# Kernel optimization log

Measured on AMD Instinct MI355X. Metric: run time of the kernel, lower is better.

## Reference

```python
import jax, jax.numpy as jnp
import numpy as np

MARGIN = 5.0
VAR_FLOOR = 1e-4
BIG = 1e6


def setup_inputs() -> dict:
    key = jax.random.key(0)
    ks = jax.random.split(key, 8)
    B, D, R = 512, 768, 128
    C_new, C_old = 10, 100
    return {
        "features": jax.random.normal(ks[0], (B, D), jnp.float32),
        "labels": jax.random.randint(ks[1], (B,), 0, C_new),
        "new_class_ids": jnp.arange(C_new),
        "cur_means": jax.random.normal(ks[2], (C_new, D), jnp.float32),
        "cur_bases": jax.random.normal(ks[3], (C_new, D, R), jnp.float32),
        "cur_variances": jax.random.uniform(ks[4], (C_new, R + 1), jnp.float32),
        "calibrated_old_means": jax.random.normal(ks[5], (C_old, D), jnp.float32),
        "calibrated_old_bases": jax.random.normal(ks[6], (C_old, D, R), jnp.float32),
        "calibrated_old_variances": jax.random.uniform(ks[7], (C_old, R + 1), jnp.float32),
    }


def _geometry_distance_matrix(z, means, bases, variances):
    # z: [B,D], means: [C,D], bases: [C,D,R], variances: [C,R+1] -> [B,C]
    diff = z[:, None, :] - means[None, :, :]                    # [B,C,D]
    coeff = jnp.einsum('bcd,cdr->bcr', diff, bases)             # [B,C,R]
    eig = jnp.maximum(variances[:, :-1], VAR_FLOOR)             # [C,R]
    res = jnp.maximum(variances[:, -1], VAR_FLOOR)              # [C]
    parallel = jnp.sum(coeff * coeff / eig[None, :, :], axis=-1)  # [B,C]
    recon = jnp.einsum('bcr,cdr->bcd', coeff, bases)            # [B,C,D]
    residual_term = jnp.sum((diff - recon) ** 2, axis=-1) / res[None, :]
    dist = (parallel + residual_term) / z.shape[1]              # normalize_by_dim
    return jnp.nan_to_num(dist, nan=BIG, posinf=BIG, neginf=BIG)


def reference(features, labels, new_class_ids, cur_means, cur_bases, cur_variances,
              calibrated_old_means, calibrated_old_bases, calibrated_old_variances):
    z = jnp.nan_to_num(features, nan=0.0, posinf=0.0, neginf=0.0)  # [B,D]
    labels = labels.reshape(-1)

    own_all = _geometry_distance_matrix(z, cur_means, cur_bases, cur_variances)  # [B,C_new_total]
    old_all = _geometry_distance_matrix(z, calibrated_old_means, calibrated_old_bases,
                                        calibrated_old_variances)               # [B,C_old]
    old_min = jnp.min(old_all, axis=1)                                           # [B]

    # Per-new-class masks; union of class masks reproduces new_mask implicitly.
    masks = (labels[None, :] == new_class_ids[:, None]).astype(z.dtype)          # [K,B]
    counts = masks.sum(axis=1)                                                   # [K]
    denom = jnp.maximum(counts, 1.0)

    own_k = own_all[:, new_class_ids].T                                          # [K,B]
    hinge = jax.nn.relu(MARGIN + own_k - old_min[None, :])                       # [K,B]

    total_k = (hinge * masks).sum(axis=1) / denom
    own_k_mean = (own_k * masks).sum(axis=1) / denom
    old_k_mean = (old_min[None, :] * masks).sum(axis=1) / denom

    valid = (counts > 0).astype(z.dtype)
    n_valid = jnp.maximum(valid.sum(), 1.0)
    total = (total_k * valid).sum() / n_valid
    own = (own_k_mean * valid).sum() / n_valid
    old = (old_k_mean * valid).sum() / n_valid
    return jnp.stack([total, own, old])  # [total, own, old]
```

## Files before the change

kernel.cpp:

```cpp
#include <hip/hip_runtime.h>
#include <hip/hip_bf16.h>
#include <math.h>
#include <stdint.h>

#define B_N   512
#define D_N   768
#define R_N   128
#define C_NEW 10
#define C_OLD 100
#define C_TOT 110
#define MARGIN_F    5.0f
#define VAR_FLOOR_F 1e-4f
#define BIG_F       1e6f

typedef __bf16 bf16;
typedef __bf16 bf16x4 __attribute__((ext_vector_type(4)));
typedef __bf16 bf16x8 __attribute__((ext_vector_type(8)));
typedef float  f32x4  __attribute__((ext_vector_type(4)));

__device__ __forceinline__ float cleanf(float v) { return isfinite(v) ? v : 0.0f; }

__device__ __forceinline__ unsigned encf(float f) {
    unsigned u = __float_as_uint(f);
    return (u & 0x80000000u) ? ~u : (u | 0x80000000u);
}
__device__ __forceinline__ float decf(unsigned u) {
    return (u & 0x80000000u) ? __uint_as_float(u & 0x7fffffffu) : __uint_as_float(~u);
}

__global__ __launch_bounds__(256)
void prep_T(const float* __restrict__ cur_bases, const float* __restrict__ old_bases,
            bf16* __restrict__ basesT, unsigned* __restrict__ ominE,
            unsigned* __restrict__ cnt)
{
    const int bid = blockIdx.x, t = threadIdx.x;
    if (bid == 0) {
        ominE[t] = 0xFFFFFFFFu;
        ominE[256 + t] = 0xFFFFFFFFu;
        if (t == 0) *cnt = 0u;
    }

    const int dt = bid % 6, c = bid / 6;
    const float* Bc = (c < C_NEW) ? cur_bases + (size_t)c * D_N * R_N
                                  : old_bases + (size_t)(c - C_NEW) * D_N * R_N;
    __shared__ bf16 T[128][128];
    const int d0 = dt * 128;
    const int rg  = t & 31;
    const int dgb = t >> 5;

    #pragma unroll
    for (int i = 0; i < 4; ++i) {
        const int dg = i * 8 + dgb;
        const float* src = Bc + (size_t)(d0 + dg * 4) * R_N + rg * 4;
        float4 v0 = *(const float4*)(src);
        float4 v1 = *(const float4*)(src + R_N);
        float4 v2 = *(const float4*)(src + 2 * R_N);
        float4 v3 = *(const float4*)(src + 3 * R_N);
        const float* f0 = (const float*)&v0;
        const float* f1 = (const float*)&v1;
        const float* f2 = (const float*)&v2;
        const float* f3 = (const float*)&v3;
        #pragma unroll
        for (int j = 0; j < 4; ++j) {
            const int R = rg * 4 + j;
            const int pc = dg ^ (R & 31);
            bf16x4 w;
            w[0] = (bf16)f0[j]; w[1] = (bf16)f1[j]; w[2] = (bf16)f2[j]; w[3] = (bf16)f3[j];
            *(bf16x4*)(&T[R][pc * 4]) = w;
        }
    }
    __syncthreads();

    #pragma unroll
    for (int it = 0; it < 16; ++it) {
        const int q = it * 256 + t;
        const int r = q >> 5, u = q & 31;
        const int pc = u ^ (r & 31);
        ushort4 w = *(const ushort4*)(&T[r][pc * 4]);
        *(ushort4*)(basesT + (size_t)c * R_N * D_N + (size_t)r * D_N + d0 + u * 4) = w;
    }
}

#define PADC 136
#define SM_A   0
#define SM_B   18432
#define SM_C   0
#define SM_G   36864
#define SM_MU  71680
#define SM_INV 74752
#define SM_Q   75264
#define SM_PAR 75776
#define SM_CN  76288
#define SM_ND  76800
#define SM_T2  77312
#define SM_FL  79360
#define SM_SZ  79376

__global__ __launch_bounds__(256, 2)
void main_all(const float* __restrict__ z, const bf16* __restrict__ basesT,
              const float* __restrict__ cur_vars, const float* __restrict__ old_vars,
              const float* __restrict__ cur_means, const float* __restrict__ old_means,
              const int* __restrict__ labels, const int* __restrict__ ncid,
              float* __restrict__ gdist, unsigned* __restrict__ ominE,
              unsigned* __restrict__ cnt, float* __restrict__ out)
{
    __shared__ __align__(16) unsigned char smem[SM_SZ];
    bf16*  sA   = (bf16*)(smem + SM_A);
    bf16*  sB   = (bf16*)(smem + SM_B);
    bf16*  sC   = (bf16*)(smem + SM_C);
    bf16*  sG   = (bf16*)(smem + SM_G);
    float* sMu  = (float*)(smem + SM_MU);
    float* sInv = (float*)(smem + SM_INV);
    float* sQ   = (float*)(smem + SM_Q);
    float* sPar = (float*)(smem + SM_PAR);
    float* sCn  = (float*)(smem + SM_CN);
    float* sNd  = (float*)(smem + SM_ND);
    float* sT2  = (float*)(smem + SM_T2);
    unsigned* sFl = (unsigned*)(smem + SM_FL);

    const int tid = threadIdx.x, wave = tid >> 6, lane = tid & 63;
    const int quad = lane >> 4, l15 = lane & 15;
    const int wr = (wave >> 1) * 64, wc = (wave & 1) * 64;

    const int fid = blockIdx.x;
    const int c  = (fid & 7) + 8 * (fid >> 5);
    const int mt = (fid >> 3) & 3;

    if (c < C_TOT) {
        const int b0 = mt * 128;
        const float* vars = (c < C_NEW) ? cur_vars + (size_t)c * (R_N + 1)
                                        : old_vars + (size_t)(c - C_NEW) * (R_N + 1);
        const float* mu = (c < C_NEW) ? cur_means + (size_t)c * D_N
                                      : old_means + (size_t)(c - C_NEW) * D_N;

        if (tid < 128) {
            sInv[tid] = 1.0f / fmaxf(vars[tid], VAR_FLOOR_F);
            sQ[tid] = 0.0f;
        }
        for (int i = tid; i < D_N; i += 256) sMu[i] = mu[i];

        f32x4 acc1[4][4], accG[4][4];
        #pragma unroll
        for (int i = 0; i < 4; ++i)
            #pragma unroll
            for (int j = 0; j < 4; ++j) { acc1[i][j] = (f32x4)0.0f; accG[i][j] = (f32x4)0.0f; }
        float nd2p[8];
        #pragma unroll
        for (int p = 0; p < 8; ++p) nd2p[p] = 0.f;

        const int rb = tid >> 4, f4 = tid & 15;
        const float* Az = z + (size_t)b0 * D_N;
        const bf16*  Bb = basesT + (size_t)c * R_N * D_N;

        for (int k0 = 0; k0 < D_N; k0 += 64) {
            __syncthreads();
            #pragma unroll
            for (int p = 0; p < 4; ++p) {
                int q = p * 256 + tid, row = q >> 3, u = q & 7;
                *(uint4*)(sB + row * 72 + u * 8) = *(const uint4*)(Bb + (size_t)row * D_N + k0 + u * 8);
            }
            {
                float4 m4 = *(const float4*)(sMu + k0 + f4 * 4);
                #pragma unroll
                for (int p = 0; p < 8; ++p) {
                    int row = p * 16 + rb;
                    float4 v = *(const float4*)(Az + (size_t)row * D_N + k0 + f4 * 4);
                    float d0 = cleanf(v.x) - m4.x;
                    float d1 = cleanf(v.y) - m4.y;
                    float d2 = cleanf(v.z) - m4.z;
                    float d3 = cleanf(v.w) - m4.w;
                    nd2p[p] += d0 * d0 + d1 * d1 + d2 * d2 + d3 * d3;
                    bf16x4 w;
                    w[0] = (bf16)d0; w[1] = (bf16)d1; w[2] = (bf16)d2; w[3] = (bf16)d3;
                    *(bf16x4*)(sA + row * 72 + f4 * 4) = w;
                }
            }
            __syncthreads();
            #pragma unroll
            for (int kk = 0; kk < 64; kk += 32) {
                bf16x8 afA[4], bgB[4], afB[4];
                #pragma unroll
                for (int i = 0; i < 4; ++i) afA[i] = *(const bf16x8*)(sA + (wr + 16 * i + l15) * 72 + kk + quad * 8);
                #pragma unroll
                for (int j = 0; j < 4; ++j) bgB[j] = *(const bf16x8*)(sB + (wc + 16 * j + l15) * 72 + kk + quad * 8);
                #pragma unroll
                for (int i = 0; i < 4; ++i) afB[i] = *(const bf16x8*)(sB + (wr + 16 * i + l15) * 72 + kk + quad * 8);
                #pragma unroll
                for (int i = 0; i < 4; ++i)
                    #pragma unroll
                    for (int j = 0; j < 4; ++j) {
                        acc1[i][j] = __builtin_amdgcn_mfma_f32_16x16x32_bf16(afA[i], bgB[j], acc1[i][j], 0, 0, 0);
                        accG[i][j] = __builtin_amdgcn_mfma_f32_16x16x32_bf16(afB[i], bgB[j], accG[i][j], 0, 0, 0);
                    }
            }
        }

        #pragma unroll
        for (int p = 0; p < 8; ++p) {
            float s = nd2p[p];
            s += __shfl_xor(s, 1, 64); s += __shfl_xor(s, 2, 64);
            s += __shfl_xor(s, 4, 64); s += __shfl_xor(s, 8, 64);
            if (l15 == 0) sNd[p * 16 + rb] = s;
        }

        #pragma unroll
        for (int i = 0; i < 4; ++i)
            #pragma unroll
            for (int j = 0; j < 4; ++j)
                #pragma unroll
                for (int reg = 0; reg < 4; ++reg)
                    sG[(wr + 16 * i + quad * 4 + reg) * PADC + wc + 16 * j + l15] = (bf16)accG[i][j][reg];
        __syncthreads();

        #pragma unroll
        for (int i = 0; i < 4; ++i)
            #pragma unroll
            for (int j = 0; j < 4; ++j)
                #pragma unroll
                for (int reg = 0; reg < 4; ++reg)
                    sC[(wr + 16 * i + quad * 4 + reg) * PADC + wc + 16 * j + l15] = (bf16)acc1[i][j][reg];
        __syncthreads();

        {
            int row = tid >> 1, half = tid & 1;
            float par = 0.f, cn = 0.f;
            #pragma unroll
            for (int m = 0; m < 8; ++m) {
                bf16x8 v = *(const bf16x8*)(sC + row * PADC + half * 64 + m * 8);
                #pragma unroll
                for (int e = 0; e < 8; ++e) {
                    float f = (float)v[e];
                    int col = half * 64 + m * 8 + e;
                    cn  += f * f;
                    par += f * f * sInv[col];
                }
            }
            sT2[tid] = par;
            sT2[256 + tid] = cn;
        }
        __syncthreads();
        if (tid < 128) {
            sPar[tid] = sT2[tid * 2] + sT2[tid * 2 + 1];
            sCn[tid]  = sT2[256 + tid * 2] + sT2[256 + tid * 2 + 1];
        }

        f32x4 acc2[4][4];
        #pragma unroll
        for (int i = 0; i < 4; ++i)
            #pragma unroll
            for (int j = 0; j < 4; ++j) acc2[i][j] = (f32x4)0.0f;
        #pragma unroll
        for (int kc = 0; kc < 128; kc += 32) {
            bf16x8 af[4], bg[4];
            #pragma unroll
            for (int i = 0; i < 4; ++i) af[i] = *(const bf16x8*)(sC + (wr + 16 * i + l15) * PADC + kc + quad * 8);
            #pragma unroll
            for (int j = 0; j < 4; ++j) bg[j] = *(const bf16x8*)(sG + (wc + 16 * j + l15) * PADC + kc + quad * 8);
            #pragma unroll
            for (int i = 0; i < 4; ++i)
                #pragma unroll
                for (int j = 0; j < 4; ++j)
                    acc2[i][j] = __builtin_amdgcn_mfma_f32_16x16x32_bf16(af[i], bg[j], acc2[i][j], 0, 0, 0);
        }

        #pragma unroll
        for (int i = 0; i < 4; ++i)
            #pragma unroll
            for (int reg = 0; reg < 4; ++reg) {
                float qp = 0.f;
                #pragma unroll
                for (int j = 0; j < 4; ++j) qp += acc2[i][j][reg] * acc1[i][j][reg];
                qp += __shfl_xor(qp, 1, 64);
                qp += __shfl_xor(qp, 2, 64);
                qp += __shfl_xor(qp, 4, 64);
                qp += __shfl_xor(qp, 8, 64);
                if (l15 == 0) atomicAdd(&sQ[wr + 16 * i + quad * 4 + reg], qp);
            }
        __syncthreads();

        if (tid < 128) {
            int b = b0 + tid;
            float res = fmaxf(vars[R_N], VAR_FLOOR_F);
            float dist = (sPar[tid] + (sNd[tid] - 2.0f * sCn[tid] + sQ[tid]) / res) / (float)D_N;
            if (!isfinite(dist)) dist = BIG_F;
            if (c < C_NEW) {
                gdist[(size_t)b * C_NEW + c] = dist;
            } else {
                atomicMin(ominE + b, encf(dist));
            }
        }
    }

    __syncthreads();
    if (tid == 0) {
        __threadfence();
        sFl[0] = atomicAdd(cnt, 1u);
    }
    __syncthreads();
    if (sFl[0] == 447u) {
        __threadfence();
        float* accF = sT2;
        int* ncidS = (int*)(sT2 + 48);
        if (tid < 40) accF[tid] = 0.f;
        if (tid < C_NEW) ncidS[tid] = ncid[tid];
        __syncthreads();
        #pragma unroll
        for (int rep = 0; rep < 2; ++rep) {
            int b = rep * 256 + tid;
            float mn = decf(ominE[b]);
            int lab = labels[b];
            #pragma unroll
            for (int k = 0; k < C_NEW; ++k) {
                if (lab == ncidS[k]) {
                    int col = min(max(ncidS[k], 0), C_NEW - 1);
                    float ow = gdist[(size_t)b * C_NEW + col];
                    atomicAdd(&accF[k * 4 + 0], 1.0f);
                    atomicAdd(&accF[k * 4 + 1], fmaxf(0.0f, MARGIN_F + ow - mn));
                    atomicAdd(&accF[k * 4 + 2], ow);
                    atomicAdd(&accF[k * 4 + 3], mn);
                }
            }
        }
        __syncthreads();
        if (tid == 0) {
            float total = 0.f, own = 0.f, old = 0.f, nv = 0.f;
            #pragma unroll
            for (int k = 0; k < C_NEW; ++k) {
                float cntk = accF[k * 4 + 0];
                float den = fmaxf(cntk, 1.0f);
                if (cntk > 0.f) {
                    nv += 1.f;
                    total += accF[k * 4 + 1] / den;
                    own   += accF[k * 4 + 2] / den;
                    old   += accF[k * 4 + 3] / den;
                }
            }
            float nvd = fmaxf(nv, 1.0f);
            out[0] = total / nvd;
            out[1] = own / nvd;
            out[2] = old / nvd;
        }
    }
}

extern "C" void kernel_launch(void* const* d_in, const int* in_sizes, int n_in,
                              void* d_out, int out_size, void* d_ws, size_t ws_size,
                              hipStream_t stream)
{
    const float* features  = (const float*)d_in[0];
    const int*   labels    = (const int*)d_in[1];
    const int*   ncid      = (const int*)d_in[2];
    const float* cur_means = (const float*)d_in[3];
    const float* cur_bases = (const float*)d_in[4];
    const float* cur_vars  = (const float*)d_in[5];
    const float* old_means = (const float*)d_in[6];
    const float* old_bases = (const float*)d_in[7];
    const float* old_vars  = (const float*)d_in[8];

    unsigned char* ws = (unsigned char*)d_ws;
    float*    gdist  = (float*)(ws + 0);
    unsigned* ominE  = (unsigned*)(ws + 20480);
    unsigned* cnt    = (unsigned*)(ws + 22528);
    bf16*     basesT = (bf16*) (ws + 22544);

    prep_T<<<dim3(6 * C_TOT), dim3(256), 0, stream>>>(cur_bases, old_bases,
                                                      basesT, ominE, cnt);
    main_all<<<dim3(448), dim3(256), 0, stream>>>(features, basesT,
                                                  cur_vars, old_vars,
                                                  cur_means, old_means,
                                                  labels, ncid,
                                                  gdist, ominE, cnt, (float*)d_out);
}
```

Measured before the change: 165.5 us.

## Split Gram and projection GEMM loops with register prefetch; move finalize to separate kernel

The fused K loop that computed both the projection (diff·B) and the Gram matrix (BᵀB) is split into two sequential 12-step loops. Each loop prefetches the next chunk of bases and features into registers while the current chunk is in shared memory, so global loads overlap the MFMA work. The last-block atomic counter reduction is replaced by a separate single-block finalize kernel, and blocks with no class now return early. Running two loops reads the bases tile twice and holds more live registers for the prefetch buffers, which may reduce occupancy under launch_bounds(256,2), and it adds one kernel launch.

```diff
diff --git a/kernel.cpp b/kernel.cpp
--- a/kernel.cpp
+++ b/kernel.cpp
@@ -30,14 +30,12 @@
 
 __global__ __launch_bounds__(256)
 void prep_T(const float* __restrict__ cur_bases, const float* __restrict__ old_bases,
-            bf16* __restrict__ basesT, unsigned* __restrict__ ominE,
-            unsigned* __restrict__ cnt)
+            bf16* __restrict__ basesT, unsigned* __restrict__ ominE)
 {
     const int bid = blockIdx.x, t = threadIdx.x;
     if (bid == 0) {
         ominE[t] = 0xFFFFFFFFu;
         ominE[256 + t] = 0xFFFFFFFFu;
-        if (t == 0) *cnt = 0u;
     }
 
     const int dt = bid % 6, c = bid / 6;
@@ -93,17 +91,19 @@
 #define SM_CN  76288
 #define SM_ND  76800
 #define SM_T2  77312
-#define SM_FL  79360
-#define SM_SZ  79376
+#define SM_SZ  79360
 
 __global__ __launch_bounds__(256, 2)
 void main_all(const float* __restrict__ z, const bf16* __restrict__ basesT,
               const float* __restrict__ cur_vars, const float* __restrict__ old_vars,
               const float* __restrict__ cur_means, const float* __restrict__ old_means,
-              const int* __restrict__ labels, const int* __restrict__ ncid,
-              float* __restrict__ gdist, unsigned* __restrict__ ominE,
-              unsigned* __restrict__ cnt, float* __restrict__ out)
+              float* __restrict__ gdist, unsigned* __restrict__ ominE)
 {
+    const int fid = blockIdx.x;
+    const int c  = (fid & 7) + 8 * (fid >> 5);
+    const int mt = (fid >> 3) & 3;
+    if (c >= C_TOT) return;
+
     __shared__ __align__(16) unsigned char smem[SM_SZ];
     bf16*  sA   = (bf16*)(smem + SM_A);
     bf16*  sB   = (bf16*)(smem + SM_B);
@@ -116,230 +116,288 @@
     float* sCn  = (float*)(smem + SM_CN);
     float* sNd  = (float*)(smem + SM_ND);
     float* sT2  = (float*)(smem + SM_T2);
-    unsigned* sFl = (unsigned*)(smem + SM_FL);
 
     const int tid = threadIdx.x, wave = tid >> 6, lane = tid & 63;
     const int quad = lane >> 4, l15 = lane & 15;
     const int wr = (wave >> 1) * 64, wc = (wave & 1) * 64;
 
-    const int fid = blockIdx.x;
-    const int c  = (fid & 7) + 8 * (fid >> 5);
-    const int mt = (fid >> 3) & 3;
-
-    if (c < C_TOT) {
-        const int b0 = mt * 128;
-        const float* vars = (c < C_NEW) ? cur_vars + (size_t)c * (R_N + 1)
-                                        : old_vars + (size_t)(c - C_NEW) * (R_N + 1);
-        const float* mu = (c < C_NEW) ? cur_means + (size_t)c * D_N
-                                      : old_means + (size_t)(c - C_NEW) * D_N;
-
-        if (tid < 128) {
-            sInv[tid] = 1.0f / fmaxf(vars[tid], VAR_FLOOR_F);
-            sQ[tid] = 0.0f;
-        }
-        for (int i = tid; i < D_N; i += 256) sMu[i] = mu[i];
-
-        f32x4 acc1[4][4], accG[4][4];
-        #pragma unroll
-        for (int i = 0; i < 4; ++i)
-            #pragma unroll
-            for (int j = 0; j < 4; ++j) { acc1[i][j] = (f32x4)0.0f; accG[i][j] = (f32x4)0.0f; }
-        float nd2p[8];
-        #pragma unroll
-        for (int p = 0; p < 8; ++p) nd2p[p] = 0.f;
-
-        const int rb = tid >> 4, f4 = tid & 15;
-        const float* Az = z + (size_t)b0 * D_N;
-        const bf16*  Bb = basesT + (size_t)c * R_N * D_N;
-
-        for (int k0 = 0; k0 < D_N; k0 += 64) {
-            __syncthreads();
+    const int b0 = mt * 128;
+    const float* vars = (c < C_NEW) ? cur_vars + (size_t)c * (R_N + 1)
+                                    : old_vars + (size_t)(c - C_NEW) * (R_N + 1);
+    const float* mu = (c < C_NEW) ? cur_means + (size_t)c * D_N
+                                  : old_means + (size_t)(c - C_NEW) * D_N;
+
+    if (tid < 128) {
+        sInv[tid] = 1.0f / fmaxf(vars[tid], VAR_FLOOR_F);
+        sQ[tid] = 0.0f;
+    }
+    for (int i = tid; i < D_N; i += 256) sMu[i] = mu[i];
+
+    const int srow = (tid * 8) >> 6 , dummy = srow;
+    (void)dummy;
+    const int qrow = tid >> 3 << 0;
+    (void)qrow;
+
+    const bf16* Bb = basesT + (size_t)c * R_N * D_N;
+    const float* Az = z + (size_t)b0 * D_N;
+    const int rb = tid >> 4, f4 = tid & 15;
+
+    f32x4 accG[4][4];
+    #pragma unroll
+    for (int i = 0; i < 4; ++i)
+        #pragma unroll
+        for (int j = 0; j < 4; ++j) accG[i][j] = (f32x4)0.0f;
+
+    uint4 pb[4];
+    #pragma unroll
+    for (int p = 0; p < 4; ++p) {
+        int q = p * 256 + tid, row = q >> 3, u = q & 7;
+        pb[p] = *(const uint4*)(Bb + (size_t)row * D_N + 0 + u * 8);
+    }
+
+    for (int kc = 0; kc < 12; ++kc) {
+        __syncthreads();
+        #pragma unroll
+        for (int p = 0; p < 4; ++p) {
+            int q = p * 256 + tid, row = q >> 3, u = q & 7;
+            *(uint4*)(sB + row * 72 + u * 8) = pb[p];
+        }
+        if (kc < 11) {
             #pragma unroll
             for (int p = 0; p < 4; ++p) {
                 int q = p * 256 + tid, row = q >> 3, u = q & 7;
-                *(uint4*)(sB + row * 72 + u * 8) = *(const uint4*)(Bb + (size_t)row * D_N + k0 + u * 8);
-            }
-            {
-                float4 m4 = *(const float4*)(sMu + k0 + f4 * 4);
-                #pragma unroll
-                for (int p = 0; p < 8; ++p) {
-                    int row = p * 16 + rb;
-                    float4 v = *(const float4*)(Az + (size_t)row * D_N + k0 + f4 * 4);
-                    float d0 = cleanf(v.x) - m4.x;
-                    float d1 = cleanf(v.y) - m4.y;
-                    float d2 = cleanf(v.z) - m4.z;
-                    float d3 = cleanf(v.w) - m4.w;
-                    nd2p[p] += d0 * d0 + d1 * d1 + d2 * d2 + d3 * d3;
-                    bf16x4 w;
-                    w[0] = (bf16)d0; w[1] = (bf16)d1; w[2] = (bf16)d2; w[3] = (bf16)d3;
-                    *(bf16x4*)(sA + row * 72 + f4 * 4) = w;
-                }
-            }
-            __syncthreads();
-            #pragma unroll
-            for (int kk = 0; kk < 64; kk += 32) {
-                bf16x8 afA[4], bgB[4], afB[4];
-                #pragma unroll
-                for (int i = 0; i < 4; ++i) afA[i] = *(const bf16x8*)(sA + (wr + 16 * i + l15) * 72 + kk + quad * 8);
-                #pragma unroll
-                for (int j = 0; j < 4; ++j) bgB[j] = *(const bf16x8*)(sB + (wc + 16 * j + l15) * 72 + kk + quad * 8);
-                #pragma unroll
-                for (int i = 0; i < 4; ++i) afB[i] = *(const bf16x8*)(sB + (wr + 16 * i + l15) * 72 + kk + quad * 8);
-                #pragma unroll
-                for (int i = 0; i < 4; ++i)
-                    #pragma unroll
-                    for (int j = 0; j < 4; ++j) {
-                        acc1[i][j] = __builtin_amdgcn_mfma_f32_16x16x32_bf16(afA[i], bgB[j], acc1[i][j], 0, 0, 0);
-                        accG[i][j] = __builtin_amdgcn_mfma_f32_16x16x32_bf16(afB[i], bgB[j], accG[i][j], 0, 0, 0);
-                    }
-            }
-        }
-
-        #pragma unroll
-        for (int p = 0; p < 8; ++p) {
-            float s = nd2p[p];
-            s += __shfl_xor(s, 1, 64); s += __shfl_xor(s, 2, 64);
-            s += __shfl_xor(s, 4, 64); s += __shfl_xor(s, 8, 64);
-            if (l15 == 0) sNd[p * 16 + rb] = s;
-        }
-
-        #pragma unroll
-        for (int i = 0; i < 4; ++i)
-            #pragma unroll
-            for (int j = 0; j < 4; ++j)
-                #pragma unroll
-                for (int reg = 0; reg < 4; ++reg)
-                    sG[(wr + 16 * i + quad * 4 + reg) * PADC + wc + 16 * j + l15] = (bf16)accG[i][j][reg];
+                pb[p] = *(const uint4*)(Bb + (size_t)row * D_N + (kc + 1) * 64 + u * 8);
+            }
+        }
         __syncthreads();
-
-        #pragma unroll
-        for (int i = 0; i < 4; ++i)
-            #pragma unroll
-            for (int j = 0; j < 4; ++j)
-                #pragma unroll
-                for (int reg = 0; reg < 4; ++reg)
-                    sC[(wr + 16 * i + quad * 4 + reg) * PADC + wc + 16 * j + l15] = (bf16)acc1[i][j][reg];
-        __syncthreads();
-
-        {
-            int row = tid >> 1, half = tid & 1;
-            float par = 0.f, cn = 0.f;
-            #pragma unroll
-            for (int m = 0; m < 8; ++m) {
-                bf16x8 v = *(const bf16x8*)(sC + row * PADC + half * 64 + m * 8);
-                #pragma unroll
-                for (int e = 0; e < 8; ++e) {
-                    float f = (float)v[e];
-                    int col = half * 64 + m * 8 + e;
-                    cn  += f * f;
-                    par += f * f * sInv[col];
-                }
-            }
-            sT2[tid] = par;
-            sT2[256 + tid] = cn;
-        }
-        __syncthreads();
-        if (tid < 128) {
-            sPar[tid] = sT2[tid * 2] + sT2[tid * 2 + 1];
-            sCn[tid]  = sT2[256 + tid * 2] + sT2[256 + tid * 2 + 1];
-        }
-
-        f32x4 acc2[4][4];
-        #pragma unroll
-        for (int i = 0; i < 4; ++i)
-            #pragma unroll
-            for (int j = 0; j < 4; ++j) acc2[i][j] = (f32x4)0.0f;
-        #pragma unroll
-        for (int kc = 0; kc < 128; kc += 32) {
-            bf16x8 af[4], bg[4];
-            #pragma unroll
-            for (int i = 0; i < 4; ++i) af[i] = *(const bf16x8*)(sC + (wr + 16 * i + l15) * PADC + kc + quad * 8);
-            #pragma unroll
-            for (int j = 0; j < 4; ++j) bg[j] = *(const bf16x8*)(sG + (wc + 16 * j + l15) * PADC + kc + quad * 8);
+        #pragma unroll
+        for (int kk = 0; kk < 64; kk += 32) {
+            bf16x8 afB[4], bgB[4];
+            #pragma unroll
+            for (int i = 0; i < 4; ++i) afB[i] = *(const bf16x8*)(sB + (wr + 16 * i + l15) * 72 + kk + quad * 8);
+            #pragma unroll
+            for (int j = 0; j < 4; ++j) bgB[j] = *(const bf16x8*)(sB + (wc + 16 * j + l15) * 72 + kk + quad * 8);
             #pragma unroll
             for (int i = 0; i < 4; ++i)
                 #pragma unroll
                 for (int j = 0; j < 4; ++j)
-                    acc2[i][j] = __builtin_amdgcn_mfma_f32_16x16x32_bf16(af[i], bg[j], acc2[i][j], 0, 0, 0);
-        }
-
+                    accG[i][j] = __builtin_amdgcn_mfma_f32_16x16x32_bf16(afB[i], bgB[j], accG[i][j], 0, 0, 0);
+        }
+    }
+    #pragma unroll
+    for (int i = 0; i < 4; ++i)
+        #pragma unroll
+        for (int j = 0; j < 4; ++j)
+            #pragma unroll
+            for (int reg = 0; reg < 4; ++reg)
+                sG[(wr + 16 * i + quad * 4 + reg) * PADC + wc + 16 * j + l15] = (bf16)accG[i][j][reg];
+
+    f32x4 acc1[4][4];
+    #pragma unroll
+    for (int i = 0; i < 4; ++i)
+        #pragma unroll
+        for (int j = 0; j < 4; ++j) acc1[i][j] = (f32x4)0.0f;
+    float nd2p[8];
+    #pragma unroll
+    for (int p = 0; p < 8; ++p) nd2p[p] = 0.f;
+
+    float4 pa[8];
+    #pragma unroll
+    for (int p = 0; p < 4; ++p) {
+        int q = p * 256 + tid, row = q >> 3, u = q & 7;
+        pb[p] = *(const uint4*)(Bb + (size_t)row * D_N + 0 + u * 8);
+    }
+    #pragma unroll
+    for (int p = 0; p < 8; ++p) {
+        int row = p * 16 + rb;
+        pa[p] = *(const float4*)(Az + (size_t)row * D_N + 0 + f4 * 4);
+    }
+
+    for (int kc = 0; kc < 12; ++kc) {
+        const int k0 = kc * 64;
+        __syncthreads();
+        #pragma unroll
+        for (int p = 0; p < 4; ++p) {
+            int q = p * 256 + tid, row = q >> 3, u = q & 7;
+            *(uint4*)(sB + row * 72 + u * 8) = pb[p];
+        }
+        {
+            float4 m4 = *(const float4*)(sMu + k0 + f4 * 4);
+            #pragma unroll
+            for (int p = 0; p < 8; ++p) {
+                int row = p * 16 + rb;
+                float d0 = cleanf(pa[p].x) - m4.x;
+                float d1 = cleanf(pa[p].y) - m4.y;
+                float d2 = cleanf(pa[p].z) - m4.z;
+                float d3 = cleanf(pa[p].w) - m4.w;
+                nd2p[p] += d0 * d0 + d1 * d1 + d2 * d2 + d3 * d3;
+                bf16x4 w;
+                w[0] = (bf16)d0; w[1] = (bf16)d1; w[2] = (bf16)d2; w[3] = (bf16)d3;
+                *(bf16x4*)(sA + row * 72 + f4 * 4) = w;
+            }
+        }
+        if (kc < 11) {
+            #pragma unroll
+            for (int p = 0; p < 4; ++p) {
+                int q = p * 256 + tid, row = q >> 3, u = q & 7;
+                pb[p] = *(const uint4*)(Bb + (size_t)row * D_N + (kc + 1) * 64 + u * 8);
+            }
+            #pragma unroll
+            for (int p = 0; p < 8; ++p) {
+                int row = p * 16 + rb;
+                pa[p] = *(const float4*)(Az + (size_t)row * D_N + (kc + 1) * 64 + f4 * 4);
+            }
+        }
+        __syncthreads();
+        #pragma unroll
+        for (int kk = 0; kk < 64; kk += 32) {
+            bf16x8 afA[4], bgB[4];
+            #pragma unroll
+            for (int i = 0; i < 4; ++i) afA[i] = *(const bf16x8*)(sA + (wr + 16 * i + l15) * 72 + kk + quad * 8);
+            #pragma unroll
+            for (int j = 0; j < 4; ++j) bgB[j] = *(const bf16x8*)(sB + (wc + 16 * j + l15) * 72 + kk + quad * 8);
+            #pragma unroll
+            for (int i = 0; i < 4; ++i)
+                #pragma unroll
+                for (int j = 0; j < 4; ++j)
+                    acc1[i][j] = __builtin_amdgcn_mfma_f32_16x16x32_bf16(afA[i], bgB[j], acc1[i][j], 0, 0, 0);
+        }
+    }
+
+    #pragma unroll
+    for (int p = 0; p < 8; ++p) {
+        float s = nd2p[p];
+        s += __shfl_xor(s, 1, 64); s += __shfl_xor(s, 2, 64);
+        s += __shfl_xor(s, 4, 64); s += __shfl_xor(s, 8, 64);
+        if (l15 == 0) sNd[p * 16 + rb] = s;
+    }
+    __syncthreads();
+
+    #pragma unroll
+    for (int i = 0; i < 4; ++i)
+        #pragma unroll
+        for (int j = 0; j < 4; ++j)
+            #pragma unroll
+            for (int reg = 0; reg < 4; ++reg)
+                sC[(wr + 16 * i + quad * 4 + reg) * PADC + wc + 16 * j + l15] = (bf16)acc1[i][j][reg];
+    __syncthreads();
+
+    {
+        int row = tid >> 1, half = tid & 1;
+        float par = 0.f, cn = 0.f;
+        #pragma unroll
+        for (int m = 0; m < 8; ++m) {
+            bf16x8 v = *(const bf16x8*)(sC + row * PADC + half * 64 + m * 8);
+            #pragma unroll
+            for (int e = 0; e < 8; ++e) {
+                float f = (float)v[e];
+                int col = half * 64 + m * 8 + e;
+                cn  += f * f;
+                par += f * f * sInv[col];
+            }
+        }
+        sT2[tid] = par;
+        sT2[256 + tid] = cn;
+    }
+    __syncthreads();
+    if (tid < 128) {
+        sPar[tid] = sT2[tid * 2] + sT2[tid * 2 + 1];
+        sCn[tid]  = sT2[256 + tid * 2] + sT2[256 + tid * 2 + 1];
+    }
+
+    f32x4 acc2[4][4];
+    #pragma unroll
+    for (int i = 0; i < 4; ++i)
+        #pragma unroll
+        for (int j = 0; j < 4; ++j) acc2[i][j] = (f32x4)0.0f;
+    #pragma unroll
+    for (int kc = 0; kc < 128; kc += 32) {
+        bf16x8 af[4], bg[4];
+        #pragma unroll
+        for (int i = 0; i < 4; ++i) af[i] = *(const bf16x8*)(sC + (wr + 16 * i + l15) * PADC + kc + quad * 8);
+        #pragma unroll
+        for (int j = 0; j < 4; ++j) bg[j] = *(const bf16x8*)(sG + (wc + 16 * j + l15) * PADC + kc + quad * 8);
         #pragma unroll
         for (int i = 0; i < 4; ++i)
             #pragma unroll
-            for (int reg = 0; reg < 4; ++reg) {
-                float qp = 0.f;
-                #pragma unroll
-                for (int j = 0; j < 4; ++j) qp += acc2[i][j][reg] * acc1[i][j][reg];
-                qp += __shfl_xor(qp, 1, 64);
-                qp += __shfl_xor(qp, 2, 64);
-                qp += __shfl_xor(qp, 4, 64);
-                qp += __shfl_xor(qp, 8, 64);
-                if (l15 == 0) atomicAdd(&sQ[wr + 16 * i + quad * 4 + reg], qp);
-            }
-        __syncthreads();
-
-        if (tid < 128) {
-            int b = b0 + tid;
-            float res = fmaxf(vars[R_N], VAR_FLOOR_F);
-            float dist = (sPar[tid] + (sNd[tid] - 2.0f * sCn[tid] + sQ[tid]) / res) / (float)D_N;
-            if (!isfinite(dist)) dist = BIG_F;
-            if (c < C_NEW) {
-                gdist[(size_t)b * C_NEW + c] = dist;
-            } else {
-                atomicMin(ominE + b, encf(dist));
-            }
-        }
-    }
-
-    __syncthreads();
-    if (tid == 0) {
-        __threadfence();
-        sFl[0] = atomicAdd(cnt, 1u);
-    }
-    __syncthreads();
-    if (sFl[0] == 447u) {
-        __threadfence();
-        float* accF = sT2;
-        int* ncidS = (int*)(sT2 + 48);
-        if (tid < 40) accF[tid] = 0.f;
-        if (tid < C_NEW) ncidS[tid] = ncid[tid];
-        __syncthreads();
-        #pragma unroll
-        for (int rep = 0; rep < 2; ++rep) {
-            int b = rep * 256 + tid;
-            float mn = decf(ominE[b]);
-            int lab = labels[b];
-            #pragma unroll
-            for (int k = 0; k < C_NEW; ++k) {
-                if (lab == ncidS[k]) {
-                    int col = min(max(ncidS[k], 0), C_NEW - 1);
-                    float ow = gdist[(size_t)b * C_NEW + col];
-                    atomicAdd(&accF[k * 4 + 0], 1.0f);
-                    atomicAdd(&accF[k * 4 + 1], fmaxf(0.0f, MARGIN_F + ow - mn));
-                    atomicAdd(&accF[k * 4 + 2], ow);
-                    atomicAdd(&accF[k * 4 + 3], mn);
-                }
-            }
-        }
-        __syncthreads();
-        if (tid == 0) {
-            float total = 0.f, own = 0.f, old = 0.f, nv = 0.f;
-            #pragma unroll
-            for (int k = 0; k < C_NEW; ++k) {
-                float cntk = accF[k * 4 + 0];
-                float den = fmaxf(cntk, 1.0f);
-                if (cntk > 0.f) {
-                    nv += 1.f;
-                    total += accF[k * 4 + 1] / den;
-                    own   += accF[k * 4 + 2] / den;
-                    old   += accF[k * 4 + 3] / den;
-                }
-            }
-            float nvd = fmaxf(nv, 1.0f);
-            out[0] = total / nvd;
-            out[1] = own / nvd;
-            out[2] = old / nvd;
-        }
+            for (int j = 0; j < 4; ++j)
+                acc2[i][j] = __builtin_amdgcn_mfma_f32_16x16x32_bf16(af[i], bg[j], acc2[i][j], 0, 0, 0);
+    }
+
+    #pragma unroll
+    for (int i = 0; i < 4; ++i)
+        #pragma unroll
+        for (int reg = 0; reg < 4; ++reg) {
+            float qp = 0.f;
+            #pragma unroll
+            for (int j = 0; j < 4; ++j) qp += acc2[i][j][reg] * acc1[i][j][reg];
+            qp += __shfl_xor(qp, 1, 64);
+            qp += __shfl_xor(qp, 2, 64);
+            qp += __shfl_xor(qp, 4, 64);
+            qp += __shfl_xor(qp, 8, 64);
+            if (l15 == 0) atomicAdd(&sQ[wr + 16 * i + quad * 4 + reg], qp);
+        }
+    __syncthreads();
+
+    if (tid < 128) {
+        int b = b0 + tid;
+        float res = fmaxf(vars[R_N], VAR_FLOOR_F);
+        float dist = (sPar[tid] + (sNd[tid] - 2.0f * sCn[tid] + sQ[tid]) / res) / (float)D_N;
+        if (!isfinite(dist)) dist = BIG_F;
+        if (c < C_NEW) {
+            gdist[(size_t)b * C_NEW + c] = dist;
+        } else {
+            atomicMin(ominE + b, encf(dist));
+        }
+    }
+}
+
+__global__ __launch_bounds__(512)
+void finalize(const float* __restrict__ gdist, const unsigned* __restrict__ ominE,
+              const int* __restrict__ labels, const int* __restrict__ ncid,
+              float* __restrict__ out)
+{
+    __shared__ float acc[C_NEW * 4];
+    __shared__ int sNcid[C_NEW];
+    const int t = threadIdx.x;
+    if (t < C_NEW * 4) acc[t] = 0.f;
+    if (t < C_NEW) sNcid[t] = ncid[t];
+    __syncthreads();
+
+    {
+        float mn = decf(ominE[t]);
+        const int lab = labels[t];
+        #pragma unroll
+        for (int k = 0; k < C_NEW; ++k) {
+            if (lab == sNcid[k]) {
+                int col = min(max(sNcid[k], 0), C_NEW - 1);
+                float ow = gdist[(size_t)t * C_NEW + col];
+                atomicAdd(&acc[k * 4 + 0], 1.0f);
+                atomicAdd(&acc[k * 4 + 1], fmaxf(0.0f, MARGIN_F + ow - mn));
+                atomicAdd(&acc[k * 4 + 2], ow);
+                atomicAdd(&acc[k * 4 + 3], mn);
+            }
+        }
+    }
+    __syncthreads();
+
+    if (t == 0) {
+        float total = 0.f, own = 0.f, old = 0.f, nv = 0.f;
+        #pragma unroll
+        for (int k = 0; k < C_NEW; ++k) {
+            float cnt = acc[k * 4 + 0];
+            float den = fmaxf(cnt, 1.0f);
+            if (cnt > 0.f) {
+                nv += 1.f;
+                total += acc[k * 4 + 1] / den;
+                own   += acc[k * 4 + 2] / den;
+                old   += acc[k * 4 + 3] / den;
+            }
+        }
+        float nvd = fmaxf(nv, 1.0f);
+        out[0] = total / nvd;
+        out[1] = own / nvd;
+        out[2] = old / nvd;
     }
 }
 
@@ -360,14 +418,14 @@
     unsigned char* ws = (unsigned char*)d_ws;
     float*    gdist  = (float*)(ws + 0);
     unsigned* ominE  = (unsigned*)(ws + 20480);
-    unsigned* cnt    = (unsigned*)(ws + 22528);
-    bf16*     basesT = (bf16*) (ws + 22544);
+    bf16*     basesT = (bf16*) (ws + 22528);
 
     prep_T<<<dim3(6 * C_TOT), dim3(256), 0, stream>>>(cur_bases, old_bases,
-                                                      basesT, ominE, cnt);
+                                                      basesT, ominE);
     main_all<<<dim3(448), dim3(256), 0, stream>>>(features, basesT,
                                                   cur_vars, old_vars,
                                                   cur_means, old_means,
-                                                  labels, ncid,
-                                                  gdist, ominE, cnt, (float*)d_out);
-}
+                                                  gdist, ominE);
+    finalize<<<dim3(1), dim3(512), 0, stream>>>(gdist, ominE, labels, ncid,
+                                                (float*)d_out);
+}
```

Measured after the change: 186.5 us. +12.7%, slower.
